# Performance work log

Measured on AMD Instinct MI355X. Metric: run time of the kernel, lower is better.

The kernel has to match this reference:

```python
import jax, jax.numpy as jnp
import numpy as np

HIDDEN = 512
BATCH = 32
SEQ = 4096


def setup_inputs() -> dict:
    key = jax.random.key(0)
    k1, k2, k3, k4, k5 = jax.random.split(key, 5)
    s = 1.0 / np.sqrt(2 * HIDDEN)
    return {
        "hidden": jax.random.normal(k1, (BATCH, HIDDEN), dtype=jnp.float32),
        "encoder_outputs": jax.random.normal(k2, (BATCH, SEQ, HIDDEN), dtype=jnp.float32),
        "attn_w": jax.random.uniform(k3, (HIDDEN, 2 * HIDDEN), dtype=jnp.float32, minval=-s, maxval=s),
        "attn_b": jax.random.uniform(k4, (HIDDEN,), dtype=jnp.float32, minval=-s, maxval=s),
        "v_w": jax.random.uniform(k5, (1, HIDDEN), dtype=jnp.float32, minval=-1.0 / np.sqrt(HIDDEN), maxval=1.0 / np.sqrt(HIDDEN)),
    }


def reference(hidden, encoder_outputs, attn_w, attn_b, v_w):
    # attn_w maps concat([hidden_repeated, encoder_outputs]) of size 2H -> H.
    # Split into the hidden part and encoder part to avoid materializing the concat.
    H = hidden.shape[-1]
    Wh = attn_w[:, :H]   # [H, H] applied to repeated hidden
    We = attn_w[:, H:]   # [H, H] applied to encoder outputs
    # hidden contribution is constant over seq_len: [B, 1, H]
    h_proj = jnp.einsum("bh,kh->bk", hidden, Wh)[:, None, :] + attn_b
    e_proj = jnp.einsum("bsh,kh->bsk", encoder_outputs, We)
    energy = jnp.tanh(h_proj + e_proj)                       # [B, S, H]
    scores = jnp.einsum("bsk,k->bs", energy, v_w[0])          # [B, S]
    return jax.nn.softmax(scores, axis=1)
```

## Files before the change

kernel.cpp:

```cpp
#include <hip/hip_runtime.h>

#define HIDDEN 512
#define SEQN 4096
#define BM 128
#define BK 64

typedef __attribute__((ext_vector_type(8))) short short8;
typedef __attribute__((ext_vector_type(4))) float f32x4;

__device__ __forceinline__ short f2bf(float f) {
  unsigned u = __float_as_uint(f);
  u = u + 0x7FFFu + ((u >> 16) & 1u);
  return (short)(u >> 16);
}

__global__ void k_convW(const float* __restrict__ attn_w, short* __restrict__ wbf) {
  int i = blockIdx.x * 256 + threadIdx.x;
  int f = i * 4;
  int k = f >> 9;
  int h = f & 511;
  const float4 v = *reinterpret_cast<const float4*>(attn_w + k * 1024 + 512 + h);
  short o[4] = { f2bf(v.x), f2bf(v.y), f2bf(v.z), f2bf(v.w) };
  *reinterpret_cast<uint2*>(wbf + f) = *reinterpret_cast<const uint2*>(o);
}

__global__ void k_hproj(const float* __restrict__ hidden, const float* __restrict__ attn_w,
                        const float* __restrict__ attn_b, float* __restrict__ hp) {
  int b = blockIdx.y;
  int k = blockIdx.x * 128 + threadIdx.x;
  __shared__ float hsh[HIDDEN];
  *reinterpret_cast<float4*>(hsh + threadIdx.x * 4) =
      *reinterpret_cast<const float4*>(hidden + b * HIDDEN + threadIdx.x * 4);
  __syncthreads();
  const float* wr = attn_w + k * 1024;
  float s = attn_b[k];
  #pragma unroll 8
  for (int h = 0; h < HIDDEN; h += 4) {
    float4 wv = *reinterpret_cast<const float4*>(wr + h);
    s += wv.x * hsh[h] + wv.y * hsh[h + 1] + wv.z * hsh[h + 2] + wv.w * hsh[h + 3];
  }
  hp[b * HIDDEN + k] = s;
}

__global__ __launch_bounds__(512, 2) void k_main(
    const float* __restrict__ enc, const short* __restrict__ wbf,
    const float* __restrict__ hp, const float* __restrict__ vw,
    float* __restrict__ scores) {
  __shared__ __align__(16) short A_ls[BM * BK];
  __shared__ float part[8][BM];

  const int tid = threadIdx.x;
  const int w = tid >> 6;
  const int l = tid & 63;
  const int lq = l >> 4;
  const int lr = l & 15;

  const int bid = blockIdx.x;
  const int b = bid >> 5;
  const int s0 = (bid & 31) * BM;
  const float* encB = enc + ((size_t)b * SEQN + s0) * HIDDEN;

  const int r0 = tid >> 3;
  const int cg = tid & 7;
  const int wa0 = r0 * 64 + ((cg * 8) ^ ((r0 & 7) << 3));
  const int wa1 = (r0 + 64) * 64 + ((cg * 8) ^ ((r0 & 7) << 3));

  const short* wBase = wbf + (w * 64 + lr) * HIDDEN + lq * 8;

  f32x4 acc[8][4];
  #pragma unroll
  for (int mi = 0; mi < 8; ++mi)
    #pragma unroll
    for (int ni = 0; ni < 4; ++ni)
      acc[mi][ni] = (f32x4){0.f, 0.f, 0.f, 0.f};

  float4 ga0, ga1, gb0, gb1;
  {
    const float* p0 = encB + r0 * HIDDEN + cg * 8;
    const float* p1 = encB + (r0 + 64) * HIDDEN + cg * 8;
    ga0 = *reinterpret_cast<const float4*>(p0);
    ga1 = *reinterpret_cast<const float4*>(p0 + 4);
    gb0 = *reinterpret_cast<const float4*>(p1);
    gb1 = *reinterpret_cast<const float4*>(p1 + 4);
  }

  for (int st = 0; st < 8; ++st) {
    __syncthreads();
    {
      short8 o0, o1;
      o0[0]=f2bf(ga0.x); o0[1]=f2bf(ga0.y); o0[2]=f2bf(ga0.z); o0[3]=f2bf(ga0.w);
      o0[4]=f2bf(ga1.x); o0[5]=f2bf(ga1.y); o0[6]=f2bf(ga1.z); o0[7]=f2bf(ga1.w);
      o1[0]=f2bf(gb0.x); o1[1]=f2bf(gb0.y); o1[2]=f2bf(gb0.z); o1[3]=f2bf(gb0.w);
      o1[4]=f2bf(gb1.x); o1[5]=f2bf(gb1.y); o1[6]=f2bf(gb1.z); o1[7]=f2bf(gb1.w);
      *reinterpret_cast<short8*>(A_ls + wa0) = o0;
      *reinterpret_cast<short8*>(A_ls + wa1) = o1;
    }
    __syncthreads();
    if (st < 7) {
      const float* p0 = encB + r0 * HIDDEN + (st + 1) * BK + cg * 8;
      const float* p1 = encB + (r0 + 64) * HIDDEN + (st + 1) * BK + cg * 8;
      ga0 = *reinterpret_cast<const float4*>(p0);
      ga1 = *reinterpret_cast<const float4*>(p0 + 4);
      gb0 = *reinterpret_cast<const float4*>(p1);
      gb1 = *reinterpret_cast<const float4*>(p1 + 4);
    }
    short8 wf[2][4];
    #pragma unroll
    for (int kk = 0; kk < 2; ++kk)
      #pragma unroll
      for (int ni = 0; ni < 4; ++ni)
        wf[kk][ni] = *reinterpret_cast<const short8*>(wBase + ni * (16 * HIDDEN) + st * BK + kk * 32);
    #pragma unroll
    for (int kk = 0; kk < 2; ++kk) {
      short8 af[8];
      #pragma unroll
      for (int mi = 0; mi < 8; ++mi)
        af[mi] = *reinterpret_cast<const short8*>(
            A_ls + (mi * 16 + lr) * 64 + ((kk * 32 + lq * 8) ^ ((lr & 7) << 3)));
      #pragma unroll
      for (int mi = 0; mi < 8; ++mi)
        #pragma unroll
        for (int ni = 0; ni < 4; ++ni)
          acc[mi][ni] = __builtin_amdgcn_mfma_f32_16x16x32_bf16(af[mi], wf[kk][ni], acc[mi][ni], 0, 0, 0);
    }
  }

  float hpv[4], vv[4];
  {
    const float* hpb = hp + b * HIDDEN;
    const int colb = w * 64 + lr;
    #pragma unroll
    for (int ni = 0; ni < 4; ++ni) {
      hpv[ni] = hpb[colb + ni * 16];
      vv[ni]  = vw[colb + ni * 16];
    }
  }
  float rp[8][4];
  #pragma unroll
  for (int mi = 0; mi < 8; ++mi)
    #pragma unroll
    for (int r = 0; r < 4; ++r) {
      float s = 0.f;
      #pragma unroll
      for (int ni = 0; ni < 4; ++ni) {
        float x = acc[mi][ni][r] + hpv[ni];
        float e = __expf(2.0f * x);
        float th = 1.0f - 2.0f / (e + 1.0f);
        s += th * vv[ni];
      }
      rp[mi][r] = s;
    }
  #pragma unroll
  for (int mk = 1; mk <= 8; mk <<= 1)
    #pragma unroll
    for (int mi = 0; mi < 8; ++mi)
      #pragma unroll
      for (int r = 0; r < 4; ++r)
        rp[mi][r] += __shfl_xor(rp[mi][r], mk, 64);
  if (lr == 0) {
    #pragma unroll
    for (int mi = 0; mi < 8; ++mi)
      #pragma unroll
      for (int r = 0; r < 4; ++r)
        part[w][mi * 16 + lq * 4 + r] = rp[mi][r];
  }
  __syncthreads();
  if (tid < BM) {
    float s = 0.f;
    #pragma unroll
    for (int ww = 0; ww < 8; ++ww) s += part[ww][tid];
    scores[b * SEQN + s0 + tid] = s;
  }
}

__global__ void k_softmax(const float* __restrict__ scores, float* __restrict__ out) {
  const int b = blockIdx.x;
  const int t = threadIdx.x;
  const float* row = scores + b * SEQN;
  float4 x[4];
  #pragma unroll
  for (int i = 0; i < 4; ++i)
    x[i] = *reinterpret_cast<const float4*>(row + (i * 256 + t) * 4);
  float m = -1e30f;
  #pragma unroll
  for (int i = 0; i < 4; ++i)
    m = fmaxf(m, fmaxf(fmaxf(x[i].x, x[i].y), fmaxf(x[i].z, x[i].w)));
  #pragma unroll
  for (int mk = 1; mk < 64; mk <<= 1) m = fmaxf(m, __shfl_xor(m, mk, 64));
  __shared__ float redmax[4], redsum[4];
  if ((t & 63) == 0) redmax[t >> 6] = m;
  __syncthreads();
  m = fmaxf(fmaxf(redmax[0], redmax[1]), fmaxf(redmax[2], redmax[3]));
  float sum = 0.f;
  #pragma unroll
  for (int i = 0; i < 4; ++i) {
    x[i].x = __expf(x[i].x - m); sum += x[i].x;
    x[i].y = __expf(x[i].y - m); sum += x[i].y;
    x[i].z = __expf(x[i].z - m); sum += x[i].z;
    x[i].w = __expf(x[i].w - m); sum += x[i].w;
  }
  #pragma unroll
  for (int mk = 1; mk < 64; mk <<= 1) sum += __shfl_xor(sum, mk, 64);
  if ((t & 63) == 0) redsum[t >> 6] = sum;
  __syncthreads();
  sum = redsum[0] + redsum[1] + redsum[2] + redsum[3];
  float inv = 1.0f / sum;
  #pragma unroll
  for (int i = 0; i < 4; ++i) {
    float4 o = { x[i].x * inv, x[i].y * inv, x[i].z * inv, x[i].w * inv };
    *reinterpret_cast<float4*>(out + b * SEQN + (i * 256 + t) * 4) = o;
  }
}

extern "C" void kernel_launch(void* const* d_in, const int* in_sizes, int n_in,
                              void* d_out, int out_size, void* d_ws, size_t ws_size,
                              hipStream_t stream) {
  const float* hidden = (const float*)d_in[0];
  const float* enc    = (const float*)d_in[1];
  const float* attn_w = (const float*)d_in[2];
  const float* attn_b = (const float*)d_in[3];
  const float* vw     = (const float*)d_in[4];
  float* out = (float*)d_out;

  short* wbf    = (short*)d_ws;
  float* hp     = (float*)((char*)d_ws + 512 * 1024);
  float* scores = (float*)((char*)d_ws + 512 * 1024 + 64 * 1024);

  k_convW<<<256, 256, 0, stream>>>(attn_w, wbf);
  k_hproj<<<dim3(4, 32), 128, 0, stream>>>(hidden, attn_w, attn_b, hp);
  k_main<<<1024, 512, 0, stream>>>(enc, wbf, hp, vw, scores);
  k_softmax<<<32, 256, 0, stream>>>(scores, out);
}
```

Measured before the change: 464.2 us.

## Double-buffer LDS tile in main GEMM and use packed bf16 conversion

Switches the encoder tile staging to a two-buffer LDS scheme, so the next tile is converted and stored after the MFMAs on the current buffer. This cuts the barriers per K-step from two to one. It also replaces the manual round-to-nearest bf16 conversion with the hardware v_cvt_pk_bf16_f32 instruction and fully unrolls the K loop. The changes trade doubled LDS usage and higher register and code size pressure for less barrier stalling and fewer ALU ops. The hproj kernel also gets split accumulators.

```diff
diff --git a/kernel.cpp b/kernel.cpp
--- a/kernel.cpp
+++ b/kernel.cpp
@@ -12,6 +12,12 @@
   unsigned u = __float_as_uint(f);
   u = u + 0x7FFFu + ((u >> 16) & 1u);
   return (short)(u >> 16);
+}
+
+__device__ __forceinline__ unsigned cvtpk(float a, float b) {
+  unsigned r;
+  asm("v_cvt_pk_bf16_f32 %0, %1, %2" : "=v"(r) : "v"(a), "v"(b));
+  return r;
 }
 
 __global__ void k_convW(const float* __restrict__ attn_w, short* __restrict__ wbf) {
@@ -20,8 +26,8 @@
   int k = f >> 9;
   int h = f & 511;
   const float4 v = *reinterpret_cast<const float4*>(attn_w + k * 1024 + 512 + h);
-  short o[4] = { f2bf(v.x), f2bf(v.y), f2bf(v.z), f2bf(v.w) };
-  *reinterpret_cast<uint2*>(wbf + f) = *reinterpret_cast<const uint2*>(o);
+  uint2 o = { cvtpk(v.x, v.y), cvtpk(v.z, v.w) };
+  *reinterpret_cast<uint2*>(wbf + f) = o;
 }
 
 __global__ void k_hproj(const float* __restrict__ hidden, const float* __restrict__ attn_w,
@@ -33,20 +39,23 @@
       *reinterpret_cast<const float4*>(hidden + b * HIDDEN + threadIdx.x * 4);
   __syncthreads();
   const float* wr = attn_w + k * 1024;
-  float s = attn_b[k];
+  float4 s4 = {0.f, 0.f, 0.f, 0.f};
   #pragma unroll 8
   for (int h = 0; h < HIDDEN; h += 4) {
     float4 wv = *reinterpret_cast<const float4*>(wr + h);
-    s += wv.x * hsh[h] + wv.y * hsh[h + 1] + wv.z * hsh[h + 2] + wv.w * hsh[h + 3];
-  }
-  hp[b * HIDDEN + k] = s;
+    s4.x += wv.x * hsh[h];
+    s4.y += wv.y * hsh[h + 1];
+    s4.z += wv.z * hsh[h + 2];
+    s4.w += wv.w * hsh[h + 3];
+  }
+  hp[b * HIDDEN + k] = attn_b[k] + ((s4.x + s4.y) + (s4.z + s4.w));
 }
 
 __global__ __launch_bounds__(512, 2) void k_main(
     const float* __restrict__ enc, const short* __restrict__ wbf,
     const float* __restrict__ hp, const float* __restrict__ vw,
     float* __restrict__ scores) {
-  __shared__ __align__(16) short A_ls[BM * BK];
+  __shared__ __align__(16) short A_ls[2][BM * BK];
   __shared__ float part[8][BM];
 
   const int tid = threadIdx.x;
@@ -77,52 +86,70 @@
   float4 ga0, ga1, gb0, gb1;
   {
     const float* p0 = encB + r0 * HIDDEN + cg * 8;
-    const float* p1 = encB + (r0 + 64) * HIDDEN + cg * 8;
+    const float* p1 = p0 + 64 * HIDDEN;
     ga0 = *reinterpret_cast<const float4*>(p0);
     ga1 = *reinterpret_cast<const float4*>(p0 + 4);
     gb0 = *reinterpret_cast<const float4*>(p1);
     gb1 = *reinterpret_cast<const float4*>(p1 + 4);
   }
-
+  {
+    uint4 u0 = { cvtpk(ga0.x, ga0.y), cvtpk(ga0.z, ga0.w), cvtpk(ga1.x, ga1.y), cvtpk(ga1.z, ga1.w) };
+    uint4 u1 = { cvtpk(gb0.x, gb0.y), cvtpk(gb0.z, gb0.w), cvtpk(gb1.x, gb1.y), cvtpk(gb1.z, gb1.w) };
+    *reinterpret_cast<uint4*>(&A_ls[0][wa0]) = u0;
+    *reinterpret_cast<uint4*>(&A_ls[0][wa1]) = u1;
+  }
+  __syncthreads();
+
+  #pragma unroll
   for (int st = 0; st < 8; ++st) {
-    __syncthreads();
-    {
-      short8 o0, o1;
-      o0[0]=f2bf(ga0.x); o0[1]=f2bf(ga0.y); o0[2]=f2bf(ga0.z); o0[3]=f2bf(ga0.w);
-      o0[4]=f2bf(ga1.x); o0[5]=f2bf(ga1.y); o0[6]=f2bf(ga1.z); o0[7]=f2bf(ga1.w);
-      o1[0]=f2bf(gb0.x); o1[1]=f2bf(gb0.y); o1[2]=f2bf(gb0.z); o1[3]=f2bf(gb0.w);
-      o1[4]=f2bf(gb1.x); o1[5]=f2bf(gb1.y); o1[6]=f2bf(gb1.z); o1[7]=f2bf(gb1.w);
-      *reinterpret_cast<short8*>(A_ls + wa0) = o0;
-      *reinterpret_cast<short8*>(A_ls + wa1) = o1;
-    }
-    __syncthreads();
+    const int cur = st & 1;
     if (st < 7) {
       const float* p0 = encB + r0 * HIDDEN + (st + 1) * BK + cg * 8;
-      const float* p1 = encB + (r0 + 64) * HIDDEN + (st + 1) * BK + cg * 8;
+      const float* p1 = p0 + 64 * HIDDEN;
       ga0 = *reinterpret_cast<const float4*>(p0);
       ga1 = *reinterpret_cast<const float4*>(p0 + 4);
       gb0 = *reinterpret_cast<const float4*>(p1);
       gb1 = *reinterpret_cast<const float4*>(p1 + 4);
     }
-    short8 wf[2][4];
-    #pragma unroll
-    for (int kk = 0; kk < 2; ++kk)
-      #pragma unroll
-      for (int ni = 0; ni < 4; ++ni)
-        wf[kk][ni] = *reinterpret_cast<const short8*>(wBase + ni * (16 * HIDDEN) + st * BK + kk * 32);
-    #pragma unroll
-    for (int kk = 0; kk < 2; ++kk) {
+    short8 wf0[4], wf1[4];
+    #pragma unroll
+    for (int ni = 0; ni < 4; ++ni)
+      wf0[ni] = *reinterpret_cast<const short8*>(wBase + ni * (16 * HIDDEN) + st * BK);
+    #pragma unroll
+    for (int ni = 0; ni < 4; ++ni)
+      wf1[ni] = *reinterpret_cast<const short8*>(wBase + ni * (16 * HIDDEN) + st * BK + 32);
+
+    {
       short8 af[8];
       #pragma unroll
       for (int mi = 0; mi < 8; ++mi)
         af[mi] = *reinterpret_cast<const short8*>(
-            A_ls + (mi * 16 + lr) * 64 + ((kk * 32 + lq * 8) ^ ((lr & 7) << 3)));
+            &A_ls[cur][(mi * 16 + lr) * 64 + ((lq * 8) ^ ((lr & 7) << 3))]);
       #pragma unroll
       for (int mi = 0; mi < 8; ++mi)
         #pragma unroll
         for (int ni = 0; ni < 4; ++ni)
-          acc[mi][ni] = __builtin_amdgcn_mfma_f32_16x16x32_bf16(af[mi], wf[kk][ni], acc[mi][ni], 0, 0, 0);
-    }
+          acc[mi][ni] = __builtin_amdgcn_mfma_f32_16x16x32_bf16(af[mi], wf0[ni], acc[mi][ni], 0, 0, 0);
+    }
+    {
+      short8 af[8];
+      #pragma unroll
+      for (int mi = 0; mi < 8; ++mi)
+        af[mi] = *reinterpret_cast<const short8*>(
+            &A_ls[cur][(mi * 16 + lr) * 64 + ((32 + lq * 8) ^ ((lr & 7) << 3))]);
+      #pragma unroll
+      for (int mi = 0; mi < 8; ++mi)
+        #pragma unroll
+        for (int ni = 0; ni < 4; ++ni)
+          acc[mi][ni] = __builtin_amdgcn_mfma_f32_16x16x32_bf16(af[mi], wf1[ni], acc[mi][ni], 0, 0, 0);
+    }
+    if (st < 7) {
+      uint4 u0 = { cvtpk(ga0.x, ga0.y), cvtpk(ga0.z, ga0.w), cvtpk(ga1.x, ga1.y), cvtpk(ga1.z, ga1.w) };
+      uint4 u1 = { cvtpk(gb0.x, gb0.y), cvtpk(gb0.z, gb0.w), cvtpk(gb1.x, gb1.y), cvtpk(gb1.z, gb1.w) };
+      *reinterpret_cast<uint4*>(&A_ls[cur ^ 1][wa0]) = u0;
+      *reinterpret_cast<uint4*>(&A_ls[cur ^ 1][wa1]) = u1;
+    }
+    __syncthreads();
   }
 
   float hpv[4], vv[4];
```

New measurement: 464.6 us. Within noise of the previous version (+0.1%).
